# Kernel optimization log

Measured on AMD Instinct MI355X. Metric: run time of the kernel, lower is better.

The kernel has to match this reference:

```python
import jax, jax.numpy as jnp
import numpy as np

N_NODES = 100000
N_EDGES = 400000
HIDDEN = 128
HEADS = 8
HEAD_DIM = HIDDEN // HEADS


def _lin_params(key, d_in, d_out):
    kw, kb = jax.random.split(key)
    s = 1.0 / np.sqrt(d_in)
    W = jax.random.uniform(kw, (d_in, d_out), jnp.float32, -s, s)
    b = jax.random.uniform(kb, (d_out,), jnp.float32, -s, s)
    return W, b


def setup_inputs() -> dict:
    key = jax.random.key(0)
    ks = jax.random.split(key, 12)
    inp = {
        "x": jax.random.normal(ks[0], (N_NODES, HIDDEN), jnp.float32),
        "edge_attr": jax.random.normal(ks[1], (N_EDGES, HIDDEN), jnp.float32),
        "edge_index": jax.random.randint(ks[2], (2, N_EDGES), 0, N_NODES, dtype=jnp.int32),
        "batch": jnp.zeros((N_NODES,), jnp.int32),
    }
    names = ["Q", "K", "V", "Ew", "Eb", "Ev", "O", "Eo"]
    for i, nm in enumerate(names):
        W, b = _lin_params(ks[3 + i], HIDDEN, HIDDEN)
        inp[f"W_{nm}"] = W
        inp[f"b_{nm}"] = b
    WA, bA = _lin_params(ks[11], HIDDEN, HEADS)
    inp["W_A"] = WA
    inp["b_A"] = bA
    return inp


def signed_sqrt(x):
    return jnp.sign(x) * jnp.sqrt(jnp.abs(x) + 1e-8)


def reference(x, edge_attr, edge_index, batch,
              W_Q, b_Q, W_K, b_K, W_V, b_V,
              W_Ew, b_Ew, W_Eb, b_Eb, W_Ev, b_Ev,
              W_O, b_O, W_Eo, b_Eo, W_A, b_A):
    n = x.shape[0]
    e = edge_index.shape[1]
    h, hd = HEADS, HEAD_DIM
    src, tgt = edge_index[0], edge_index[1]

    Q = (x @ W_Q + b_Q).reshape(n, h, hd)
    K = (x @ W_K + b_K).reshape(n, h, hd)
    V = (x @ W_V + b_V).reshape(n, h, hd)

    # edge-gathered attention features [E, H, HD]
    attn_feat = Q[src] + K[tgt]
    E_w = (edge_attr @ W_Ew + b_Ew).reshape(e, h, hd)
    E_b = (edge_attr @ W_Eb + b_Eb).reshape(e, h, hd)
    attn_feat = signed_sqrt(attn_feat * E_w) + E_b
    attn_feat = jax.nn.relu(attn_feat)

    # per-head scores [E, H], segment softmax over target node
    scores = attn_feat.reshape(e, h * hd) @ W_A + b_A
    seg_max = jax.ops.segment_max(scores, tgt, num_segments=n)
    ex = jnp.exp(scores - seg_max[tgt])
    seg_sum = jax.ops.segment_sum(ex, tgt, num_segments=n)
    alpha = ex / (seg_sum[tgt] + 1e-16)  # [E, H]

    a = alpha[:, :, None]
    E_v = (edge_attr @ W_Ev + b_Ev).reshape(e, h, hd)
    messages = V[src] * a + E_v * a  # [E, H, HD]

    agg = jax.ops.segment_sum(messages, tgt, num_segments=n).reshape(n, h * hd)
    x_out = agg @ W_O + b_O
    edge_attr_out = attn_feat.reshape(e, h * hd) @ W_Eo + b_Eo
    return x_out, edge_attr_out
```

## Files before the change

### kernel.cpp

```cpp
#include <hip/hip_runtime.h>
#include <hip/hip_bf16.h>

typedef __hip_bfloat16 bf16;

#define N_NODES 100000
#define N_EDGES 400000
#define EO_MIN  100000

#define OUT_E_ELEM ((size_t)N_NODES*128)
#define SCORES_B   ((size_t)N_EDGES*8*4)
#define SEG_B      ((size_t)N_NODES*8*4)
#define AGG_BYTES  ((size_t)N_NODES*128*4)
#define WSW_OFF    (SCORES_B + 2*SEG_B)

#define WT_SZ   16384
#define OFF_WQ  (0*WT_SZ)
#define OFF_WK  (2*WT_SZ)
#define OFF_WEW (4*WT_SZ)
#define OFF_WEB (6*WT_SZ)
#define OFF_WEO (8*WT_SZ)
#define OFF_WV  (10*WT_SZ)
#define OFF_WA  (12*WT_SZ)
#define WSW_SHORTS (12*WT_SZ + 2*2048)
#define WSW_BYTES  ((size_t)WSW_SHORTS*2)

using short8 = __attribute__((ext_vector_type(8))) short;
using f32x4  = __attribute__((ext_vector_type(4))) float;

__device__ __forceinline__ float b2f(bf16 v){ return __bfloat162float(v); }
__device__ __forceinline__ bf16  f2b(float v){ return __float2bfloat16(v); }
__device__ __forceinline__ short bits(bf16 v){ short s; __builtin_memcpy(&s, &v, 2); return s; }
__device__ __forceinline__ void split(float v, short& h, short& l){
  bf16 hb = f2b(v);
  h = bits(hb);
  l = bits(f2b(v - b2f(hb)));
}
__device__ __forceinline__ float san(float v){
  return (v == v && fabsf(v) < 1e30f) ? v : 0.f;
}
__device__ __forceinline__ unsigned fmap(float f){
  unsigned u = __float_as_uint(f);
  return (u & 0x80000000u) ? ~u : (u | 0x80000000u);
}
__device__ __forceinline__ float funmap(unsigned u){
  unsigned b = (u & 0x80000000u) ? (u ^ 0x80000000u) : ~u;
  return __uint_as_float(b);
}

__global__ void prep_v15(const float* __restrict__ W_Q, const float* __restrict__ W_K,
                         const float* __restrict__ W_Ew, const float* __restrict__ W_Eb,
                         const float* __restrict__ W_Eo, const float* __restrict__ W_V,
                         const float* __restrict__ W_A, short* __restrict__ wsw)
{
  const int b = blockIdx.x;
  if (b < 768){
    const int mi = b >> 7, n = b & 127;
    const float* W = (mi==0)?W_Q:(mi==1)?W_K:(mi==2)?W_Ew:(mi==3)?W_Eb:(mi==4)?W_Eo:W_V;
    short* dh = wsw + mi*2*WT_SZ;
    short* dl = dh + WT_SZ;
    for (int k = threadIdx.x; k < 128; k += 128){
      short h, l; split(W[(size_t)k*128 + n], h, l);
      dh[n*128 + k] = h; dl[n*128 + k] = l;
    }
  } else {
    const int n = b - 768;
    short* dh = wsw + OFF_WA;
    short* dl = dh + 2048;
    for (int k = threadIdx.x; k < 128; k += 128){
      float v = (n < 8) ? W_A[(size_t)k*8 + n] : 0.f;
      short h, l; split(v, h, l);
      dh[n*128 + k] = h; dl[n*128 + k] = l;
    }
  }
}

__device__ __forceinline__ void stage_row(const float* __restrict__ src,
                                          short* __restrict__ dh, short* __restrict__ dl){
  const float4 v0 = *reinterpret_cast<const float4*>(src);
  const float4 v1 = *reinterpret_cast<const float4*>(src + 4);
  const float vv[8] = {v0.x, v0.y, v0.z, v0.w, v1.x, v1.y, v1.z, v1.w};
  short8 h, l;
  #pragma unroll
  for (int q = 0; q < 8; ++q){ short hh, ll; split(vv[q], hh, ll); h[q] = hh; l[q] = ll; }
  *reinterpret_cast<short8*>(dh) = h;
  *reinterpret_cast<short8*>(dl) = l;
}

__global__ __launch_bounds__(256) void nodeproj_v15(
    const float* __restrict__ x, const short* __restrict__ wsw,
    const float* __restrict__ b_Q, const float* __restrict__ b_K,
    const float* __restrict__ b_V,
    float* __restrict__ Qn, float* __restrict__ Kn, float* __restrict__ Vn,
    int do_v)
{
  __shared__ __align__(16) short Xh[2][2048], Xl[2][2048];
  const int tid = threadIdx.x;
  const int n0  = blockIdx.x * 32;

  {
    const int r = tid & 15, c = tid >> 4;
    #pragma unroll
    for (int rg = 0; rg < 2; ++rg)
      stage_row(x + (size_t)(n0 + rg*16 + r)*128 + c*8,
                &Xh[rg][(c*16 + r)*8], &Xl[rg][(c*16 + r)*8]);
  }
  __syncthreads();

  const int wv = tid >> 6;
  const int mi = (tid & 63) & 15;
  const int kg = (tid & 63) >> 4;

  f32x4 aQ[2][2], aK[2][2], aV[2][2];
  #pragma unroll
  for (int rg = 0; rg < 2; ++rg)
    #pragma unroll
    for (int t = 0; t < 2; ++t){
      aQ[rg][t] = (f32x4){0,0,0,0}; aK[rg][t] = (f32x4){0,0,0,0}; aV[rg][t] = (f32x4){0,0,0,0};
    }

  #pragma unroll
  for (int ks = 0; ks < 4; ++ks){
    const int ao = ((ks*4 + kg)*16 + mi)*8;
    const int kb = ks*32 + kg*8;
    short8 xh[2], xl[2];
    #pragma unroll
    for (int rg = 0; rg < 2; ++rg){
      xh[rg] = *reinterpret_cast<const short8*>(&Xh[rg][ao]);
      xl[rg] = *reinterpret_cast<const short8*>(&Xl[rg][ao]);
    }
    #pragma unroll
    for (int t = 0; t < 2; ++t){
      const int n = (wv*2 + t)*16 + mi;
      const short8 qh = *reinterpret_cast<const short8*>(&wsw[OFF_WQ + n*128 + kb]);
      const short8 ql = *reinterpret_cast<const short8*>(&wsw[OFF_WQ + WT_SZ + n*128 + kb]);
      const short8 kh = *reinterpret_cast<const short8*>(&wsw[OFF_WK + n*128 + kb]);
      const short8 kl = *reinterpret_cast<const short8*>(&wsw[OFF_WK + WT_SZ + n*128 + kb]);
      const short8 vh = *reinterpret_cast<const short8*>(&wsw[OFF_WV + n*128 + kb]);
      const short8 vl = *reinterpret_cast<const short8*>(&wsw[OFF_WV + WT_SZ + n*128 + kb]);
      #pragma unroll
      for (int rg = 0; rg < 2; ++rg){
        aQ[rg][t] = __builtin_amdgcn_mfma_f32_16x16x32_bf16(xh[rg], qh, aQ[rg][t], 0,0,0);
        aK[rg][t] = __builtin_amdgcn_mfma_f32_16x16x32_bf16(xh[rg], kh, aK[rg][t], 0,0,0);
        aQ[rg][t] = __builtin_amdgcn_mfma_f32_16x16x32_bf16(xl[rg], qh, aQ[rg][t], 0,0,0);
        aK[rg][t] = __builtin_amdgcn_mfma_f32_16x16x32_bf16(xl[rg], kh, aK[rg][t], 0,0,0);
        aQ[rg][t] = __builtin_amdgcn_mfma_f32_16x16x32_bf16(xh[rg], ql, aQ[rg][t], 0,0,0);
        aK[rg][t] = __builtin_amdgcn_mfma_f32_16x16x32_bf16(xh[rg], kl, aK[rg][t], 0,0,0);
        if (do_v){
          aV[rg][t] = __builtin_amdgcn_mfma_f32_16x16x32_bf16(xh[rg], vh, aV[rg][t], 0,0,0);
          aV[rg][t] = __builtin_amdgcn_mfma_f32_16x16x32_bf16(xl[rg], vh, aV[rg][t], 0,0,0);
          aV[rg][t] = __builtin_amdgcn_mfma_f32_16x16x32_bf16(xh[rg], vl, aV[rg][t], 0,0,0);
        }
      }
    }
  }

  #pragma unroll
  for (int rg = 0; rg < 2; ++rg)
    #pragma unroll
    for (int t = 0; t < 2; ++t){
      const int n = (wv*2 + t)*16 + mi;
      const float bq = b_Q[n], bk = b_K[n], bv = b_V[n];
      #pragma unroll
      for (int q = 0; q < 4; ++q){
        const size_t row = n0 + rg*16 + kg*4 + q;
        Qn[row*128 + n] = aQ[rg][t][q] + bq;
        Kn[row*128 + n] = aK[rg][t][q] + bk;
        if (do_v) Vn[row*128 + n] = aV[rg][t][q] + bv;
      }
    }
}

__global__ __launch_bounds__(256) void front_qk_v15(
    const float* __restrict__ ea, const int* __restrict__ eidx,
    const float* __restrict__ Qn, const float* __restrict__ Kn,
    const float* __restrict__ b_Ew, const float* __restrict__ b_Eb,
    const float* __restrict__ b_A,  const float* __restrict__ b_Eo,
    const short* __restrict__ wsw,
    float* __restrict__ scores, unsigned* __restrict__ segmax,
    float* __restrict__ oute, int eo_min, int do_score)
{
  __shared__ __align__(16) short eaAFh[2][2048], eaAFl[2][2048];
  __shared__ float qk[32][128];
  __shared__ int sIdx[32], tIdx[32];

  const int tid = threadIdx.x;
  const int e0  = blockIdx.x * 32;

  if (tid < 32){
    sIdx[tid] = eidx[e0 + tid];
    tIdx[tid] = eidx[N_EDGES + e0 + tid];
  }
  __syncthreads();

  {
    const int r = tid & 15, c = tid >> 4;
    #pragma unroll
    for (int rg = 0; rg < 2; ++rg)
      stage_row(ea + (size_t)(e0 + rg*16 + r)*128 + c*8,
                &eaAFh[rg][(c*16 + r)*8], &eaAFl[rg][(c*16 + r)*8]);
  }
  {
    const int r = tid >> 3, cg = tid & 7;
    const float* qp = Qn + (size_t)sIdx[r]*128 + cg*16;
    const float* kp = Kn + (size_t)tIdx[r]*128 + cg*16;
    #pragma unroll
    for (int p = 0; p < 4; ++p){
      const float4 qv = *reinterpret_cast<const float4*>(qp + p*4);
      const float4 kv = *reinterpret_cast<const float4*>(kp + p*4);
      float4 s; s.x = qv.x+kv.x; s.y = qv.y+kv.y; s.z = qv.z+kv.z; s.w = qv.w+kv.w;
      *reinterpret_cast<float4*>(&qk[r][cg*16 + p*4]) = s;
    }
  }
  __syncthreads();

  const int wv = tid >> 6;
  const int mi = (tid & 63) & 15;
  const int kg = (tid & 63) >> 4;

  f32x4 aw[2][2], ab[2][2];
  #pragma unroll
  for (int rg = 0; rg < 2; ++rg)
    #pragma unroll
    for (int t = 0; t < 2; ++t){ aw[rg][t] = (f32x4){0,0,0,0}; ab[rg][t] = (f32x4){0,0,0,0}; }

  #pragma unroll
  for (int ks = 0; ks < 4; ++ks){
    const int ao = ((ks*4 + kg)*16 + mi)*8;
    const int kb = ks*32 + kg*8;
    short8 eh[2], el_[2];
    #pragma unroll
    for (int rg = 0; rg < 2; ++rg){
      eh[rg]  = *reinterpret_cast<const short8*>(&eaAFh[rg][ao]);
      el_[rg] = *reinterpret_cast<const short8*>(&eaAFl[rg][ao]);
    }
    #pragma unroll
    for (int t = 0; t < 2; ++t){
      const int n = (wv*2 + t)*16 + mi;
      const short8 wh = *reinterpret_cast<const short8*>(&wsw[OFF_WEW + n*128 + kb]);
      const short8 wl = *reinterpret_cast<const short8*>(&wsw[OFF_WEW + WT_SZ + n*128 + kb]);
      const short8 bh = *reinterpret_cast<const short8*>(&wsw[OFF_WEB + n*128 + kb]);
      const short8 bl = *reinterpret_cast<const short8*>(&wsw[OFF_WEB + WT_SZ + n*128 + kb]);
      #pragma unroll
      for (int rg = 0; rg < 2; ++rg){
        aw[rg][t] = __builtin_amdgcn_mfma_f32_16x16x32_bf16(eh[rg], wh, aw[rg][t], 0,0,0);
        ab[rg][t] = __builtin_amdgcn_mfma_f32_16x16x32_bf16(eh[rg], bh, ab[rg][t], 0,0,0);
        aw[rg][t] = __builtin_amdgcn_mfma_f32_16x16x32_bf16(el_[rg], wh, aw[rg][t], 0,0,0);
        ab[rg][t] = __builtin_amdgcn_mfma_f32_16x16x32_bf16(el_[rg], bh, ab[rg][t], 0,0,0);
        aw[rg][t] = __builtin_amdgcn_mfma_f32_16x16x32_bf16(eh[rg], wl, aw[rg][t], 0,0,0);
        ab[rg][t] = __builtin_amdgcn_mfma_f32_16x16x32_bf16(eh[rg], bl, ab[rg][t], 0,0,0);
      }
    }
  }

  short afh[2][2][4], afl[2][2][4];
  #pragma unroll
  for (int rg = 0; rg < 2; ++rg)
    #pragma unroll
    for (int t = 0; t < 2; ++t){
      const int n = (wv*2 + t)*16 + mi;
      const float bw = b_Ew[n], bb = b_Eb[n];
      #pragma unroll
      for (int q = 0; q < 4; ++q){
        const float qkv = qk[rg*16 + kg*4 + q][n];
        const float ew  = aw[rg][t][q] + bw;
        const float eb  = ab[rg][t][q] + bb;
        const float pre = qkv * ew;
        const float ssv = pre > 0.f ?  sqrtf( pre + 1e-8f)
                        : (pre < 0.f ? -sqrtf(-pre + 1e-8f) : 0.f);
        const float af = fmaxf(ssv + eb, 0.f);
        short hh, ll; split(af, hh, ll);
        afh[rg][t][q] = hh; afl[rg][t][q] = ll;
      }
    }
  __syncthreads();

  #pragma unroll
  for (int rg = 0; rg < 2; ++rg)
    #pragma unroll
    for (int t = 0; t < 2; ++t){
      const int c  = (wv*2 + t)*2 + (mi >> 3);
      const int k7 = mi & 7;
      #pragma unroll
      for (int q = 0; q < 4; ++q){
        const int idx = (c*16 + kg*4 + q)*8 + k7;
        eaAFh[rg][idx] = afh[rg][t][q];
        eaAFl[rg][idx] = afl[rg][t][q];
      }
    }
  __syncthreads();

  if (do_score && wv < 2){
    const int rg = wv;
    f32x4 acc = {0,0,0,0};
    #pragma unroll
    for (int ks = 0; ks < 4; ++ks){
      const int kb = ks*32 + kg*8;
      const int ao = ((ks*4 + kg)*16 + mi)*8;
      const short8 ah = *reinterpret_cast<const short8*>(&eaAFh[rg][ao]);
      const short8 al = *reinterpret_cast<const short8*>(&eaAFl[rg][ao]);
      const short8 bh = *reinterpret_cast<const short8*>(&wsw[OFF_WA + mi*128 + kb]);
      const short8 bl = *reinterpret_cast<const short8*>(&wsw[OFF_WA + 2048 + mi*128 + kb]);
      acc = __builtin_amdgcn_mfma_f32_16x16x32_bf16(ah, bh, acc, 0,0,0);
      acc = __builtin_amdgcn_mfma_f32_16x16x32_bf16(al, bh, acc, 0,0,0);
      acc = __builtin_amdgcn_mfma_f32_16x16x32_bf16(ah, bl, acc, 0,0,0);
    }
    if (mi < 8){
      const float ba = b_A[mi];
      #pragma unroll
      for (int q = 0; q < 4; ++q){
        const int er = rg*16 + kg*4 + q;
        const float s = san(acc[q] + ba);
        scores[(size_t)(e0 + er)*8 + mi] = s;
        atomicMax(&segmax[(size_t)tIdx[er]*8 + mi], fmap(s));
      }
    }
  }

  if (e0 >= eo_min){
    #pragma unroll
    for (int rg = 0; rg < 2; ++rg)
      #pragma unroll
      for (int t2 = 0; t2 < 2; ++t2){
        const int n = (wv*2 + t2)*16 + mi;
        f32x4 acc = {0,0,0,0};
        #pragma unroll
        for (int ks = 0; ks < 4; ++ks){
          const int kb = ks*32 + kg*8;
          const int ao = ((ks*4 + kg)*16 + mi)*8;
          const short8 ah = *reinterpret_cast<const short8*>(&eaAFh[rg][ao]);
          const short8 al = *reinterpret_cast<const short8*>(&eaAFl[rg][ao]);
          const short8 bh = *reinterpret_cast<const short8*>(&wsw[OFF_WEO + n*128 + kb]);
          const short8 bl = *reinterpret_cast<const short8*>(&wsw[OFF_WEO + WT_SZ + n*128 + kb]);
          acc = __builtin_amdgcn_mfma_f32_16x16x32_bf16(ah, bh, acc, 0,0,0);
          acc = __builtin_amdgcn_mfma_f32_16x16x32_bf16(al, bh, acc, 0,0,0);
          acc = __builtin_amdgcn_mfma_f32_16x16x32_bf16(ah, bl, acc, 0,0,0);
        }
        const float be = b_Eo[n];
        #pragma unroll
        for (int q = 0; q < 4; ++q)
          oute[(size_t)(e0 + rg*16 + kg*4 + q)*128 + n] = san(acc[q] + be);
      }
  }
}

__global__ __launch_bounds__(256) void seg_sum_v15(const float* __restrict__ scores,
    const int* __restrict__ eidx, const unsigned* __restrict__ segmax,
    float* __restrict__ segsum)
{
  int i = blockIdx.x*256 + threadIdx.x;
  if (i >= N_EDGES*8) return;
  int e = i >> 3, h = i & 7;
  int t = eidx[N_EDGES + e];
  float m = funmap(segmax[(size_t)t*8 + h]);
  atomicAdd(&segsum[(size_t)t*8 + h], expf(scores[i] - m));
}

__global__ __launch_bounds__(256) void messages_v15(
    const float* __restrict__ ea, const int* __restrict__ eidx,
    const float* __restrict__ Vn,
    const float* __restrict__ W_Ev, const float* __restrict__ b_Ev,
    const float* __restrict__ scores, const unsigned* __restrict__ segmax,
    const float* __restrict__ segsum, float* __restrict__ agg)
{
  __shared__ float eaT[128][16];
  __shared__ int sIdx[16], tIdx[16];

  const int tid = threadIdx.x;
  const int e0  = blockIdx.x * 16;

  if (tid < 16){
    sIdx[tid] = eidx[e0 + tid];
    tIdx[tid] = eidx[N_EDGES + e0 + tid];
  }
  __syncthreads();

  for (int idx = tid; idx < 16*128; idx += 256){
    int r = idx >> 7, k = idx & 127;
    eaT[k][r] = ea[(size_t)(e0 + r)*128 + k];
  }
  __syncthreads();

  const int j  = tid & 127;
  const int h8 = (tid >> 7) * 8;

  float ae[8];
  #pragma unroll
  for (int i=0;i<8;i++) ae[i] = 0.f;

  for (int k=0;k<128;k++){
    const float we = W_Ev[(size_t)k*128 + j];
    const float4 e0v = *reinterpret_cast<const float4*>(&eaT[k][h8]);
    const float4 e1v = *reinterpret_cast<const float4*>(&eaT[k][h8+4]);
    const float ev[8] = {e0v.x,e0v.y,e0v.z,e0v.w,e1v.x,e1v.y,e1v.z,e1v.w};
    #pragma unroll
    for (int i=0;i<8;i++) ae[i] = fmaf(ev[i], we, ae[i]);
  }

  const float be = b_Ev[j];
  const int h = j >> 4;
  #pragma unroll
  for (int i=0;i<8;i++){
    const int el = h8 + i;
    const size_t e = (size_t)e0 + el;
    const int t = tIdx[el];
    const float m   = funmap(segmax[(size_t)t*8 + h]);
    const float den = segsum[(size_t)t*8 + h] + 1e-16f;
    const float a   = expf(scores[e*8 + h] - m) / den;
    const float msg = san((Vn[(size_t)sIdx[el]*128 + j] + ae[i] + be) * a);
    atomicAdd(&agg[(size_t)t*128 + j], msg);
  }
}

__global__ __launch_bounds__(256) void messages_v14f(
    const float* __restrict__ x, const float* __restrict__ ea,
    const int* __restrict__ eidx,
    const float* __restrict__ W_V,  const float* __restrict__ b_V,
    const float* __restrict__ W_Ev, const float* __restrict__ b_Ev,
    const float* __restrict__ scores, const unsigned* __restrict__ segmax,
    const float* __restrict__ segsum, float* __restrict__ agg)
{
  __shared__ float eaT[128][16], xsT[128][16];
  __shared__ int sIdx[16], tIdx[16];

  const int tid = threadIdx.x;
  const int e0  = blockIdx.x * 16;

  if (tid < 16){
    sIdx[tid] = eidx[e0 + tid];
    tIdx[tid] = eidx[N_EDGES + e0 + tid];
  }
  __syncthreads();

  for (int idx = tid; idx < 16*128; idx += 256){
    int r = idx >> 7, k = idx & 127;
    eaT[k][r] = ea[(size_t)(e0 + r)*128 + k];
    xsT[k][r] = x[(size_t)sIdx[r]*128 + k];
  }
  __syncthreads();

  const int j  = tid & 127;
  const int h8 = (tid >> 7) * 8;

  float av[8], ae[8];
  #pragma unroll
  for (int i=0;i<8;i++){ av[i]=0.f; ae[i]=0.f; }

  for (int k=0;k<128;k++){
    const float wv = W_V[(size_t)k*128 + j];
    const float we = W_Ev[(size_t)k*128 + j];
    const float4 s0 = *reinterpret_cast<const float4*>(&xsT[k][h8]);
    const float4 s1 = *reinterpret_cast<const float4*>(&xsT[k][h8+4]);
    const float4 e0v = *reinterpret_cast<const float4*>(&eaT[k][h8]);
    const float4 e1v = *reinterpret_cast<const float4*>(&eaT[k][h8+4]);
    const float sv[8] = {s0.x,s0.y,s0.z,s0.w,s1.x,s1.y,s1.z,s1.w};
    const float ev[8] = {e0v.x,e0v.y,e0v.z,e0v.w,e1v.x,e1v.y,e1v.z,e1v.w};
    #pragma unroll
    for (int i=0;i<8;i++){
      av[i] = fmaf(sv[i], wv, av[i]);
      ae[i] = fmaf(ev[i], we, ae[i]);
    }
  }

  const float bv = b_V[j], be = b_Ev[j];
  const int h = j >> 4;
  #pragma unroll
  for (int i=0;i<8;i++){
    const int el = h8 + i;
    const size_t e = (size_t)e0 + el;
    const int t = tIdx[el];
    const float m   = funmap(segmax[(size_t)t*8 + h]);
    const float den = segsum[(size_t)t*8 + h] + 1e-16f;
    const float a   = expf(scores[e*8 + h] - m) / den;
    const float msg = san(((av[i] + bv) + (ae[i] + be)) * a);
    atomicAdd(&agg[(size_t)t*128 + j], msg);
  }
}

__global__ __launch_bounds__(256) void oproj_v15(const float* __restrict__ agg,
    const float* __restrict__ W, const float* __restrict__ bias,
    float* __restrict__ outx)
{
  __shared__ float AT[128][32];
  const int tid  = threadIdx.x;
  const int base = blockIdx.x * 32;

  for (int idx = tid; idx < 32*128; idx += 256){
    int r = idx >> 7, k = idx & 127;
    AT[k][r] = agg[(size_t)(base + r)*128 + k];
  }
  __syncthreads();

  const int j  = tid & 127;
  const int rb = (tid >> 7) * 16;
  float acc[16];
  #pragma unroll
  for (int i=0;i<16;i++) acc[i] = 0.f;

  for (int k=0;k<128;k++){
    const float w = W[(size_t)k*128 + j];
    const float4 a0 = *reinterpret_cast<const float4*>(&AT[k][rb]);
    const float4 a1 = *reinterpret_cast<const float4*>(&AT[k][rb+4]);
    const float4 a2 = *reinterpret_cast<const float4*>(&AT[k][rb+8]);
    const float4 a3 = *reinterpret_cast<const float4*>(&AT[k][rb+12]);
    const float avv[16] = {a0.x,a0.y,a0.z,a0.w,a1.x,a1.y,a1.z,a1.w,
                           a2.x,a2.y,a2.z,a2.w,a3.x,a3.y,a3.z,a3.w};
    #pragma unroll
    for (int i=0;i<16;i++) acc[i] = fmaf(avv[i], w, acc[i]);
  }

  const float bj = bias[j];
  #pragma unroll
  for (int i=0;i<16;i++)
    outx[(size_t)(base + rb + i)*128 + j] = san(acc[i] + bj);
}

template<bool PREPPED>
__global__ __launch_bounds__(256) void front_v14f(
    const float* __restrict__ x, const float* __restrict__ ea,
    const int* __restrict__ eidx,
    const float* __restrict__ W_Q, const float* __restrict__ b_Q,
    const float* __restrict__ W_K, const float* __restrict__ b_K,
    const float* __restrict__ W_Ew, const float* __restrict__ b_Ew,
    const float* __restrict__ W_Eb, const float* __restrict__ b_Eb,
    const float* __restrict__ b_A,
    const float* __restrict__ W_Eo, const float* __restrict__ b_Eo,
    const short* __restrict__ wsw,
    float* __restrict__ scores, unsigned* __restrict__ segmax,
    float* __restrict__ oute, int eo_min)
{
  __shared__ __align__(16) short AFh[3][2048];
  __shared__ __align__(16) short AFl[3][2048];
  __shared__ int sIdx[16], tIdx[16];

  const int tid = threadIdx.x;
  const int e0  = blockIdx.x * 16;

  if (tid < 16){
    sIdx[tid] = eidx[e0 + tid];
    tIdx[tid] = eidx[N_EDGES + e0 + tid];
  }
  __syncthreads();

  {
    const int r = tid & 15, c = tid >> 4;
    const int off = (c*16 + r)*8;
    stage_row(x  + (size_t)sIdx[r]*128 + c*8, &AFh[0][off], &AFl[0][off]);
    stage_row(x  + (size_t)tIdx[r]*128 + c*8, &AFh[1][off], &AFl[1][off]);
    stage_row(ea + (size_t)(e0 + r)*128 + c*8, &AFh[2][off], &AFl[2][off]);
  }
  __syncthreads();

  const int wv = tid >> 6;
  const int mi = (tid & 63) & 15;
  const int kg = (tid & 63) >> 4;

  f32x4 aq[2], ak[2], aw[2], ab[2];
  #pragma unroll
  for (int t = 0; t < 2; ++t){
    aq[t] = (f32x4){0,0,0,0}; ak[t] = (f32x4){0,0,0,0};
    aw[t] = (f32x4){0,0,0,0}; ab[t] = (f32x4){0,0,0,0};
  }

  #pragma unroll
  for (int ks = 0; ks < 4; ++ks){
    const int ao = ((ks*4 + kg)*16 + mi)*8;
    const short8 xh = *reinterpret_cast<const short8*>(&AFh[0][ao]);
    const short8 xl = *reinterpret_cast<const short8*>(&AFl[0][ao]);
    const short8 th = *reinterpret_cast<const short8*>(&AFh[1][ao]);
    const short8 tl = *reinterpret_cast<const short8*>(&AFl[1][ao]);
    const short8 eh = *reinterpret_cast<const short8*>(&AFh[2][ao]);
    const short8 el = *reinterpret_cast<const short8*>(&AFl[2][ao]);
    const int kb = ks*32 + kg*8;

    #pragma unroll
    for (int t = 0; t < 2; ++t){
      const int n = (wv*2 + t)*16 + mi;
      short8 qh, ql, kh, kl, wh, wl, bh, bl;
      if (PREPPED){
        qh = *reinterpret_cast<const short8*>(&wsw[OFF_WQ  + n*128 + kb]);
        ql = *reinterpret_cast<const short8*>(&wsw[OFF_WQ  + WT_SZ + n*128 + kb]);
        kh = *reinterpret_cast<const short8*>(&wsw[OFF_WK  + n*128 + kb]);
        kl = *reinterpret_cast<const short8*>(&wsw[OFF_WK  + WT_SZ + n*128 + kb]);
        wh = *reinterpret_cast<const short8*>(&wsw[OFF_WEW + n*128 + kb]);
        wl = *reinterpret_cast<const short8*>(&wsw[OFF_WEW + WT_SZ + n*128 + kb]);
        bh = *reinterpret_cast<const short8*>(&wsw[OFF_WEB + n*128 + kb]);
        bl = *reinterpret_cast<const short8*>(&wsw[OFF_WEB + WT_SZ + n*128 + kb]);
      } else {
        #pragma unroll
        for (int q = 0; q < 8; ++q){
          short h, l;
          split(W_Q [(size_t)(kb + q)*128 + n], h, l); qh[q] = h; ql[q] = l;
          split(W_K [(size_t)(kb + q)*128 + n], h, l); kh[q] = h; kl[q] = l;
          split(W_Ew[(size_t)(kb + q)*128 + n], h, l); wh[q] = h; wl[q] = l;
          split(W_Eb[(size_t)(kb + q)*128 + n], h, l); bh[q] = h; bl[q] = l;
        }
      }
      aq[t] = __builtin_amdgcn_mfma_f32_16x16x32_bf16(xh, qh, aq[t], 0,0,0);
      ak[t] = __builtin_amdgcn_mfma_f32_16x16x32_bf16(th, kh, ak[t], 0,0,0);
      aw[t] = __builtin_amdgcn_mfma_f32_16x16x32_bf16(eh, wh, aw[t], 0,0,0);
      ab[t] = __builtin_amdgcn_mfma_f32_16x16x32_bf16(eh, bh, ab[t], 0,0,0);
      aq[t] = __builtin_amdgcn_mfma_f32_16x16x32_bf16(xl, qh, aq[t], 0,0,0);
      ak[t] = __builtin_amdgcn_mfma_f32_16x16x32_bf16(tl, kh, ak[t], 0,0,0);
      aw[t] = __builtin_amdgcn_mfma_f32_16x16x32_bf16(el, wh, aw[t], 0,0,0);
      ab[t] = __builtin_amdgcn_mfma_f32_16x16x32_bf16(el, bh, ab[t], 0,0,0);
      aq[t] = __builtin_amdgcn_mfma_f32_16x16x32_bf16(xh, ql, aq[t], 0,0,0);
      ak[t] = __builtin_amdgcn_mfma_f32_16x16x32_bf16(th, kl, ak[t], 0,0,0);
      aw[t] = __builtin_amdgcn_mfma_f32_16x16x32_bf16(eh, wl, aw[t], 0,0,0);
      ab[t] = __builtin_amdgcn_mfma_f32_16x16x32_bf16(eh, bl, ab[t], 0,0,0);
    }
  }

  short afh[2][4], afl[2][4];
  #pragma unroll
  for (int t = 0; t < 2; ++t){
    const int n = (wv*2 + t)*16 + mi;
    const float bqk = b_Q[n] + b_K[n];
    const float bw  = b_Ew[n];
    const float bb  = b_Eb[n];
    #pragma unroll
    for (int q = 0; q < 4; ++q){
      const float qk = aq[t][q] + ak[t][q] + bqk;
      const float ew = aw[t][q] + bw;
      const float eb = ab[t][q] + bb;
      const float pre = qk * ew;
      const float ssv = pre > 0.f ?  sqrtf( pre + 1e-8f)
                      : (pre < 0.f ? -sqrtf(-pre + 1e-8f) : 0.f);
      const float af = fmaxf(ssv + eb, 0.f);
      short hh, ll; split(af, hh, ll);
      afh[t][q] = hh; afl[t][q] = ll;
    }
  }
  __syncthreads();

  #pragma unroll
  for (int t = 0; t < 2; ++t){
    const int c  = (wv*2 + t)*2 + (mi >> 3);
    const int k7 = mi & 7;
    #pragma unroll
    for (int q = 0; q < 4; ++q){
      const int idx = (c*16 + kg*4 + q)*8 + k7;
      AFh[0][idx] = afh[t][q];
      AFl[0][idx] = afl[t][q];
    }
  }
  __syncthreads();

  if (PREPPED && wv == 0){
    f32x4 acc = {0,0,0,0};
    #pragma unroll
    for (int ks = 0; ks < 4; ++ks){
      const int kb = ks*32 + kg*8;
      const int ao = ((ks*4 + kg)*16 + mi)*8;
      const short8 ah = *reinterpret_cast<const short8*>(&AFh[0][ao]);
      const short8 al = *reinterpret_cast<const short8*>(&AFl[0][ao]);
      const short8 bh = *reinterpret_cast<const short8*>(&wsw[OFF_WA + mi*128 + kb]);
      const short8 bl = *reinterpret_cast<const short8*>(&wsw[OFF_WA + 2048 + mi*128 + kb]);
      acc = __builtin_amdgcn_mfma_f32_16x16x32_bf16(ah, bh, acc, 0,0,0);
      acc = __builtin_amdgcn_mfma_f32_16x16x32_bf16(al, bh, acc, 0,0,0);
      acc = __builtin_amdgcn_mfma_f32_16x16x32_bf16(ah, bl, acc, 0,0,0);
    }
    if (mi < 8){
      const float ba = b_A[mi];
      #pragma unroll
      for (int q = 0; q < 4; ++q){
        const int er = kg*4 + q;
        const float s = san(acc[q] + ba);
        scores[(size_t)(e0 + er)*8 + mi] = s;
        atomicMax(&segmax[(size_t)tIdx[er]*8 + mi], fmap(s));
      }
    }
  }

  if (e0 >= eo_min){
    #pragma unroll
    for (int t2 = 0; t2 < 2; ++t2){
      const int n = (wv*2 + t2)*16 + mi;
      f32x4 acc = {0,0,0,0};
      #pragma unroll
      for (int ks = 0; ks < 4; ++ks){
        const int kb = ks*32 + kg*8;
        const int ao = ((ks*4 + kg)*16 + mi)*8;
        const short8 ah = *reinterpret_cast<const short8*>(&AFh[0][ao]);
        const short8 al = *reinterpret_cast<const short8*>(&AFl[0][ao]);
        short8 bh, bl;
        if (PREPPED){
          bh = *reinterpret_cast<const short8*>(&wsw[OFF_WEO + n*128 + kb]);
          bl = *reinterpret_cast<const short8*>(&wsw[OFF_WEO + WT_SZ + n*128 + kb]);
        } else {
          #pragma unroll
          for (int q = 0; q < 8; ++q){
            short h, l; split(W_Eo[(size_t)(kb + q)*128 + n], h, l); bh[q] = h; bl[q] = l;
          }
        }
        acc = __builtin_amdgcn_mfma_f32_16x16x32_bf16(ah, bh, acc, 0,0,0);
        acc = __builtin_amdgcn_mfma_f32_16x16x32_bf16(al, bh, acc, 0,0,0);
        acc = __builtin_amdgcn_mfma_f32_16x16x32_bf16(ah, bl, acc, 0,0,0);
      }
      const float be = b_Eo[n];
      #pragma unroll
      for (int q = 0; q < 4; ++q)
        oute[(size_t)(e0 + kg*4 + q)*128 + n] = san(acc[q] + be);
    }
  }
}

extern "C" void kernel_launch(void* const* d_in, const int* in_sizes, int n_in,
                              void* d_out, int out_size, void* d_ws, size_t ws_size,
                              hipStream_t stream)
{
  (void)in_sizes; (void)n_in; (void)out_size;
  const float* x    = (const float*)d_in[0];
  const float* ea   = (const float*)d_in[1];
  const int*   eidx = (const int*)d_in[2];
  const float* W_Q  = (const float*)d_in[4];  const float* b_Q  = (const float*)d_in[5];
  const float* W_K  = (const float*)d_in[6];  const float* b_K  = (const float*)d_in[7];
  const float* W_V  = (const float*)d_in[8];  const float* b_V  = (const float*)d_in[9];
  const float* W_Ew = (const float*)d_in[10]; const float* b_Ew = (const float*)d_in[11];
  const float* W_Eb = (const float*)d_in[12]; const float* b_Eb = (const float*)d_in[13];
  const float* W_Ev = (const float*)d_in[14]; const float* b_Ev = (const float*)d_in[15];
  const float* W_O  = (const float*)d_in[16]; const float* b_O  = (const float*)d_in[17];
  const float* W_Eo = (const float*)d_in[18]; const float* b_Eo = (const float*)d_in[19];
  const float* W_A  = (const float*)d_in[20]; const float* b_A  = (const float*)d_in[21];

  float* out_x = (float*)d_out;
  float* oute  = out_x + OUT_E_ELEM;

  float*    scores = (float*)d_out;
  unsigned* segmax = (unsigned*)((char*)d_out + SCORES_B);
  float*    segsum = (float*)((char*)d_out + SCORES_B + SEG_B);
  float*    agg    = oute;

  const size_t SZ_NODEF = (size_t)N_NODES*128*4;
  const size_t NEED_QK   = 2*SZ_NODEF + WSW_BYTES;
  const size_t NEED_FULL = 3*SZ_NODEF + WSW_BYTES;

  const int tier = (ws_size >= NEED_FULL) ? 2 : (ws_size >= NEED_QK) ? 1 : 0;

  dim3 blk(256);
  hipMemsetAsync((void*)segmax, 0, 2*SEG_B, stream);
  hipMemsetAsync((void*)agg, 0, AGG_BYTES, stream);

  if (tier >= 1){
    char*  ws  = (char*)d_ws;
    float* Qn  = (float*)ws;
    float* Kn  = (float*)(ws + SZ_NODEF);
    float* Vn  = (tier == 2) ? (float*)(ws + 2*SZ_NODEF) : nullptr;
    short* wsw = (short*)(ws + ((tier == 2) ? 3 : 2)*SZ_NODEF);

    prep_v15<<<dim3(784), dim3(128), 0, stream>>>(W_Q, W_K, W_Ew, W_Eb, W_Eo, W_V, W_A, wsw);

    nodeproj_v15<<<dim3(N_NODES/32), blk, 0, stream>>>(x, wsw, b_Q, b_K, b_V,
        Qn, Kn, Vn, tier == 2 ? 1 : 0);

    front_qk_v15<<<dim3(N_EDGES/32), blk, 0, stream>>>(ea, eidx, Qn, Kn,
        b_Ew, b_Eb, b_A, b_Eo, wsw, scores, segmax, oute, EO_MIN, 1);

    seg_sum_v15<<<dim3((N_EDGES*8 + 255)/256), blk, 0, stream>>>(scores, eidx, segmax, segsum);

    if (tier == 2)
      messages_v15<<<dim3(N_EDGES/16), blk, 0, stream>>>(ea, eidx, Vn,
          W_Ev, b_Ev, scores, segmax, segsum, agg);
    else
      messages_v14f<<<dim3(N_EDGES/16), blk, 0, stream>>>(x, ea, eidx,
          W_V, b_V, W_Ev, b_Ev, scores, segmax, segsum, agg);

    oproj_v15<<<dim3(N_NODES/32), blk, 0, stream>>>(agg, W_O, b_O, out_x);

    front_qk_v15<<<dim3(EO_MIN/32), blk, 0, stream>>>(ea, eidx, Qn, Kn,
        b_Ew, b_Eb, b_A, b_Eo, wsw, nullptr, nullptr, oute, 0, 0);

  } else {
    short* wsw = (short*)((char*)d_out + WSW_OFF);

    prep_v15<<<dim3(784), dim3(128), 0, stream>>>(W_Q, W_K, W_Ew, W_Eb, W_Eo, W_V, W_A, wsw);

    front_v14f<true><<<dim3(N_EDGES/16), blk, 0, stream>>>(x, ea, eidx,
        W_Q, b_Q, W_K, b_K, W_Ew, b_Ew, W_Eb, b_Eb, b_A, W_Eo, b_Eo, wsw,
        scores, segmax, oute, EO_MIN);

    seg_sum_v15<<<dim3((N_EDGES*8 + 255)/256), blk, 0, stream>>>(scores, eidx, segmax, segsum);

    messages_v14f<<<dim3(N_EDGES/16), blk, 0, stream>>>(x, ea, eidx,
        W_V, b_V, W_Ev, b_Ev, scores, segmax, segsum, agg);

    oproj_v15<<<dim3(N_NODES/32), blk, 0, stream>>>(agg, W_O, b_O, out_x);

    front_v14f<false><<<dim3(EO_MIN/16), blk, 0, stream>>>(x, ea, eidx,
        W_Q, b_Q, W_K, b_K, W_Ew, b_Ew, W_Eb, b_Eb, b_A, W_Eo, b_Eo, nullptr,
        nullptr, nullptr, oute, 0);
  }
}
```

Before: 1.094 ms.

## Compute E_v projection with split-bf16 MFMA and reuse Q buffer for aggregation

The messages kernel now computes the edge_attr @ W_Ev projection with bf16 hi/lo split MFMA, using a pre-swizzled W_Ev stored in the weight workspace, in place of scalar FP32 FMAs. It processes 32 edges per block. In the workspace path, aggregation now goes into the Q node buffer, which is dead after the front kernel, instead of aliasing the edge output. The front kernel can therefore write all edge outputs in one pass, and the second Eo-recompute launch is dropped. The cost is a larger weight workspace and a memset placed after the front kernel; the split-bf16 trick keeps the projection close to FP32 accuracy.

```diff
diff --git a/kernel.cpp b/kernel.cpp
--- a/kernel.cpp
+++ b/kernel.cpp
@@ -20,8 +20,9 @@
 #define OFF_WEB (6*WT_SZ)
 #define OFF_WEO (8*WT_SZ)
 #define OFF_WV  (10*WT_SZ)
-#define OFF_WA  (12*WT_SZ)
-#define WSW_SHORTS (12*WT_SZ + 2*2048)
+#define OFF_WEV (12*WT_SZ)
+#define OFF_WA  (14*WT_SZ)
+#define WSW_SHORTS (14*WT_SZ + 2*2048)
 #define WSW_BYTES  ((size_t)WSW_SHORTS*2)
 
 using short8 = __attribute__((ext_vector_type(8))) short;
@@ -47,15 +48,16 @@
   return __uint_as_float(b);
 }
 
-__global__ void prep_v15(const float* __restrict__ W_Q, const float* __restrict__ W_K,
+__global__ void prep_v16(const float* __restrict__ W_Q, const float* __restrict__ W_K,
                          const float* __restrict__ W_Ew, const float* __restrict__ W_Eb,
                          const float* __restrict__ W_Eo, const float* __restrict__ W_V,
-                         const float* __restrict__ W_A, short* __restrict__ wsw)
+                         const float* __restrict__ W_Ev, const float* __restrict__ W_A,
+                         short* __restrict__ wsw)
 {
   const int b = blockIdx.x;
-  if (b < 768){
+  if (b < 896){
     const int mi = b >> 7, n = b & 127;
-    const float* W = (mi==0)?W_Q:(mi==1)?W_K:(mi==2)?W_Ew:(mi==3)?W_Eb:(mi==4)?W_Eo:W_V;
+    const float* W = (mi==0)?W_Q:(mi==1)?W_K:(mi==2)?W_Ew:(mi==3)?W_Eb:(mi==4)?W_Eo:(mi==5)?W_V:W_Ev;
     short* dh = wsw + mi*2*WT_SZ;
     short* dl = dh + WT_SZ;
     for (int k = threadIdx.x; k < 128; k += 128){
@@ -63,7 +65,7 @@
       dh[n*128 + k] = h; dl[n*128 + k] = l;
     }
   } else {
-    const int n = b - 768;
+    const int n = b - 896;
     short* dh = wsw + OFF_WA;
     short* dl = dh + 2048;
     for (int k = threadIdx.x; k < 128; k += 128){
@@ -86,7 +88,7 @@
   *reinterpret_cast<short8*>(dl) = l;
 }
 
-__global__ __launch_bounds__(256) void nodeproj_v15(
+__global__ __launch_bounds__(256) void nodeproj_v16(
     const float* __restrict__ x, const short* __restrict__ wsw,
     const float* __restrict__ b_Q, const float* __restrict__ b_K,
     const float* __restrict__ b_V,
@@ -170,7 +172,7 @@
     }
 }
 
-__global__ __launch_bounds__(256) void front_qk_v15(
+__global__ __launch_bounds__(256) void front_qk_v16(
     const float* __restrict__ ea, const int* __restrict__ eidx,
     const float* __restrict__ Qn, const float* __restrict__ Kn,
     const float* __restrict__ b_Ew, const float* __restrict__ b_Eb,
@@ -343,7 +345,7 @@
   }
 }
 
-__global__ __launch_bounds__(256) void seg_sum_v15(const float* __restrict__ scores,
+__global__ __launch_bounds__(256) void seg_sum_v16(const float* __restrict__ scores,
     const int* __restrict__ eidx, const unsigned* __restrict__ segmax,
     float* __restrict__ segsum)
 {
@@ -355,60 +357,87 @@
   atomicAdd(&segsum[(size_t)t*8 + h], expf(scores[i] - m));
 }
 
-__global__ __launch_bounds__(256) void messages_v15(
+__global__ __launch_bounds__(256) void messages_mfma_v16(
     const float* __restrict__ ea, const int* __restrict__ eidx,
-    const float* __restrict__ Vn,
-    const float* __restrict__ W_Ev, const float* __restrict__ b_Ev,
+    const float* __restrict__ Vn, const float* __restrict__ b_Ev,
+    const short* __restrict__ wsw,
     const float* __restrict__ scores, const unsigned* __restrict__ segmax,
     const float* __restrict__ segsum, float* __restrict__ agg)
 {
-  __shared__ float eaT[128][16];
-  __shared__ int sIdx[16], tIdx[16];
+  __shared__ __align__(16) short Eh[2][2048], El[2][2048];
+  __shared__ int sIdx[32], tIdx[32];
 
   const int tid = threadIdx.x;
-  const int e0  = blockIdx.x * 16;
-
-  if (tid < 16){
+  const int e0  = blockIdx.x * 32;
+
+  if (tid < 32){
     sIdx[tid] = eidx[e0 + tid];
     tIdx[tid] = eidx[N_EDGES + e0 + tid];
   }
   __syncthreads();
 
-  for (int idx = tid; idx < 16*128; idx += 256){
-    int r = idx >> 7, k = idx & 127;
-    eaT[k][r] = ea[(size_t)(e0 + r)*128 + k];
-  }
-  __syncthreads();
-
-  const int j  = tid & 127;
-  const int h8 = (tid >> 7) * 8;
-
-  float ae[8];
-  #pragma unroll
-  for (int i=0;i<8;i++) ae[i] = 0.f;
-
-  for (int k=0;k<128;k++){
-    const float we = W_Ev[(size_t)k*128 + j];
-    const float4 e0v = *reinterpret_cast<const float4*>(&eaT[k][h8]);
-    const float4 e1v = *reinterpret_cast<const float4*>(&eaT[k][h8+4]);
-    const float ev[8] = {e0v.x,e0v.y,e0v.z,e0v.w,e1v.x,e1v.y,e1v.z,e1v.w};
-    #pragma unroll
-    for (int i=0;i<8;i++) ae[i] = fmaf(ev[i], we, ae[i]);
-  }
-
-  const float be = b_Ev[j];
-  const int h = j >> 4;
-  #pragma unroll
-  for (int i=0;i<8;i++){
-    const int el = h8 + i;
-    const size_t e = (size_t)e0 + el;
-    const int t = tIdx[el];
-    const float m   = funmap(segmax[(size_t)t*8 + h]);
-    const float den = segsum[(size_t)t*8 + h] + 1e-16f;
-    const float a   = expf(scores[e*8 + h] - m) / den;
-    const float msg = san((Vn[(size_t)sIdx[el]*128 + j] + ae[i] + be) * a);
-    atomicAdd(&agg[(size_t)t*128 + j], msg);
-  }
+  {
+    const int r = tid & 15, c = tid >> 4;
+    #pragma unroll
+    for (int rg = 0; rg < 2; ++rg)
+      stage_row(ea + (size_t)(e0 + rg*16 + r)*128 + c*8,
+                &Eh[rg][(c*16 + r)*8], &El[rg][(c*16 + r)*8]);
+  }
+  __syncthreads();
+
+  const int wv = tid >> 6;
+  const int mi = (tid & 63) & 15;
+  const int kg = (tid & 63) >> 4;
+
+  f32x4 aev[2][2];
+  #pragma unroll
+  for (int rg = 0; rg < 2; ++rg)
+    #pragma unroll
+    for (int t = 0; t < 2; ++t) aev[rg][t] = (f32x4){0,0,0,0};
+
+  #pragma unroll
+  for (int ks = 0; ks < 4; ++ks){
+    const int ao = ((ks*4 + kg)*16 + mi)*8;
+    const int kb = ks*32 + kg*8;
+    short8 eh[2], el_[2];
+    #pragma unroll
+    for (int rg = 0; rg < 2; ++rg){
+      eh[rg]  = *reinterpret_cast<const short8*>(&Eh[rg][ao]);
+      el_[rg] = *reinterpret_cast<const short8*>(&El[rg][ao]);
+    }
+    #pragma unroll
+    for (int t = 0; t < 2; ++t){
+      const int n = (wv*2 + t)*16 + mi;
+      const short8 bh = *reinterpret_cast<const short8*>(&wsw[OFF_WEV + n*128 + kb]);
+      const short8 bl = *reinterpret_cast<const short8*>(&wsw[OFF_WEV + WT_SZ + n*128 + kb]);
+      #pragma unroll
+      for (int rg = 0; rg < 2; ++rg){
+        aev[rg][t] = __builtin_amdgcn_mfma_f32_16x16x32_bf16(eh[rg], bh, aev[rg][t], 0,0,0);
+        aev[rg][t] = __builtin_amdgcn_mfma_f32_16x16x32_bf16(el_[rg], bh, aev[rg][t], 0,0,0);
+        aev[rg][t] = __builtin_amdgcn_mfma_f32_16x16x32_bf16(eh[rg], bl, aev[rg][t], 0,0,0);
+      }
+    }
+  }
+
+  #pragma unroll
+  for (int rg = 0; rg < 2; ++rg)
+    #pragma unroll
+    for (int t = 0; t < 2; ++t){
+      const int n = (wv*2 + t)*16 + mi;
+      const int h = n >> 4;
+      const float be = b_Ev[n];
+      #pragma unroll
+      for (int q = 0; q < 4; ++q){
+        const int row = rg*16 + kg*4 + q;
+        const size_t e = (size_t)e0 + row;
+        const int s = sIdx[row], tg = tIdx[row];
+        const float m   = funmap(segmax[(size_t)tg*8 + h]);
+        const float den = segsum[(size_t)tg*8 + h] + 1e-16f;
+        const float a   = expf(scores[e*8 + h] - m) / den;
+        const float msg = san((Vn[(size_t)s*128 + n] + aev[rg][t][q] + be) * a);
+        atomicAdd(&agg[(size_t)tg*128 + n], msg);
+      }
+    }
 }
 
 __global__ __launch_bounds__(256) void messages_v14f(
@@ -476,7 +505,7 @@
   }
 }
 
-__global__ __launch_bounds__(256) void oproj_v15(const float* __restrict__ agg,
+__global__ __launch_bounds__(256) void oproj_v16(const float* __restrict__ agg,
     const float* __restrict__ W, const float* __restrict__ bias,
     float* __restrict__ outx)
 {
@@ -728,7 +757,6 @@
   float*    scores = (float*)d_out;
   unsigned* segmax = (unsigned*)((char*)d_out + SCORES_B);
   float*    segsum = (float*)((char*)d_out + SCORES_B + SEG_B);
-  float*    agg    = oute;
 
   const size_t SZ_NODEF = (size_t)N_NODES*128*4;
   const size_t NEED_QK   = 2*SZ_NODEF + WSW_BYTES;
@@ -738,7 +766,6 @@
 
   dim3 blk(256);
   hipMemsetAsync((void*)segmax, 0, 2*SEG_B, stream);
-  hipMemsetAsync((void*)agg, 0, AGG_BYTES, stream);
 
   if (tier >= 1){
     char*  ws  = (char*)d_ws;
@@ -746,44 +773,47 @@
     float* Kn  = (float*)(ws + SZ_NODEF);
     float* Vn  = (tier == 2) ? (float*)(ws + 2*SZ_NODEF) : nullptr;
     short* wsw = (short*)(ws + ((tier == 2) ? 3 : 2)*SZ_NODEF);
-
-    prep_v15<<<dim3(784), dim3(128), 0, stream>>>(W_Q, W_K, W_Ew, W_Eb, W_Eo, W_V, W_A, wsw);
-
-    nodeproj_v15<<<dim3(N_NODES/32), blk, 0, stream>>>(x, wsw, b_Q, b_K, b_V,
+    float* agg = Qn;
+
+    prep_v16<<<dim3(912), dim3(128), 0, stream>>>(W_Q, W_K, W_Ew, W_Eb, W_Eo, W_V, W_Ev, W_A, wsw);
+
+    nodeproj_v16<<<dim3(N_NODES/32), blk, 0, stream>>>(x, wsw, b_Q, b_K, b_V,
         Qn, Kn, Vn, tier == 2 ? 1 : 0);
 
-    front_qk_v15<<<dim3(N_EDGES/32), blk, 0, stream>>>(ea, eidx, Qn, Kn,
-        b_Ew, b_Eb, b_A, b_Eo, wsw, scores, segmax, oute, EO_MIN, 1);
-
-    seg_sum_v15<<<dim3((N_EDGES*8 + 255)/256), blk, 0, stream>>>(scores, eidx, segmax, segsum);
+    front_qk_v16<<<dim3(N_EDGES/32), blk, 0, stream>>>(ea, eidx, Qn, Kn,
+        b_Ew, b_Eb, b_A, b_Eo, wsw, scores, segmax, oute, 0, 1);
+
+    hipMemsetAsync((void*)agg, 0, AGG_BYTES, stream);
+
+    seg_sum_v16<<<dim3((N_EDGES*8 + 255)/256), blk, 0, stream>>>(scores, eidx, segmax, segsum);
 
     if (tier == 2)
-      messages_v15<<<dim3(N_EDGES/16), blk, 0, stream>>>(ea, eidx, Vn,
-          W_Ev, b_Ev, scores, segmax, segsum, agg);
+      messages_mfma_v16<<<dim3(N_EDGES/32), blk, 0, stream>>>(ea, eidx, Vn, b_Ev,
+          wsw, scores, segmax, segsum, agg);
     else
       messages_v14f<<<dim3(N_EDGES/16), blk, 0, stream>>>(x, ea, eidx,
           W_V, b_V, W_Ev, b_Ev, scores, segmax, segsum, agg);
 
-    oproj_v15<<<dim3(N_NODES/32), blk, 0, stream>>>(agg, W_O, b_O, out_x);
-
-    front_qk_v15<<<dim3(EO_MIN/32), blk, 0, stream>>>(ea, eidx, Qn, Kn,
-        b_Ew, b_Eb, b_A, b_Eo, wsw, nullptr, nullptr, oute, 0, 0);
+    oproj_v16<<<dim3(N_NODES/32), blk, 0, stream>>>(agg, W_O, b_O, out_x);
 
   } else {
     short* wsw = (short*)((char*)d_out + WSW_OFF);
-
-    prep_v15<<<dim3(784), dim3(128), 0, stream>>>(W_Q, W_K, W_Ew, W_Eb, W_Eo, W_V, W_A, wsw);
+    float* agg = oute;
+
+    hipMemsetAsync((void*)agg, 0, AGG_BYTES, stream);
+
+    prep_v16<<<dim3(912), dim3(128), 0, stream>>>(W_Q, W_K, W_Ew, W_Eb, W_Eo, W_V, W_Ev, W_A, wsw);
 
     front_v14f<true><<<dim3(N_EDGES/16), blk, 0, stream>>>(x, ea, eidx,
         W_Q, b_Q, W_K, b_K, W_Ew, b_Ew, W_Eb, b_Eb, b_A, W_Eo, b_Eo, wsw,
         scores, segmax, oute, EO_MIN);
 
-    seg_sum_v15<<<dim3((N_EDGES*8 + 255)/256), blk, 0, stream>>>(scores, eidx, segmax, segsum);
+    seg_sum_v16<<<dim3((N_EDGES*8 + 255)/256), blk, 0, stream>>>(scores, eidx, segmax, segsum);
 
     messages_v14f<<<dim3(N_EDGES/16), blk, 0, stream>>>(x, ea, eidx,
         W_V, b_V, W_Ev, b_Ev, scores, segmax, segsum, agg);
 
-    oproj_v15<<<dim3(N_NODES/32), blk, 0, stream>>>(agg, W_O, b_O, out_x);
+    oproj_v16<<<dim3(N_NODES/32), blk, 0, stream>>>(agg, W_O, b_O, out_x);
 
     front_v14f<false><<<dim3(EO_MIN/16), blk, 0, stream>>>(x, ea, eidx,
         W_Q, b_Q, W_K, b_K, W_Ew, b_Ew, W_Eb, b_Eb, b_A, W_Eo, b_Eo, nullptr,
```

Result: faster. 972.1 us (-11.1%).
